# Performance work log

Hardware: AMD Instinct MI355X
Metric: run time of the kernel (lower is better)

Reference implementation:

```python
import jax, jax.numpy as jnp
import numpy as np

N = 50000
E = 800000
L = 0.7
EPS = 1e-12  # torch F.normalize eps


def setup_inputs() -> dict:
    key = jax.random.key(0)
    k1, k2, k3, k4, k5 = jax.random.split(key, 5)
    x = jax.random.normal(k1, (N, 256), dtype=jnp.float32)
    W = jax.random.normal(k2, (256, 128), dtype=jnp.float32) * 0.05
    b = jax.random.normal(k3, (128,), dtype=jnp.float32) * 0.05
    src = jax.random.randint(k4, (E,), 0, N, dtype=jnp.int32)
    dst = jax.random.randint(k5, (E,), 0, N, dtype=jnp.int32)
    return {"x": x, "W": W, "b": b, "src": src, "dst": dst}


def _mean_agg(h, src, dst, denom):
    # DGL copy_u + mean over in-edges: mean_{e:(u->v)} h[u]; zero for isolated nodes
    s = jax.ops.segment_sum(h[src], dst, num_segments=N)  # [N, D]
    return s / denom


def reference(x, W, b, src, dst):
    # MLP: Linear -> relu -> row-wise L2 normalize
    h = jax.nn.relu(x @ W + b)
    h = h / jnp.maximum(jnp.linalg.norm(h, axis=1, keepdims=True), EPS)
    # in-degree for mean (clamped to 1 so isolated nodes give 0, matching DGL)
    deg = jax.ops.segment_sum(jnp.ones((E,), jnp.float32), dst, num_segments=N)
    denom = jnp.maximum(deg, 1.0)[:, None]  # [N,1]
    neigh1 = _mean_agg(h, src, dst, denom)
    neigh2 = _mean_agg(neigh1, src, dst, denom)
    mean_h = L * neigh1 + (1.0 - L) * neigh2
    return (h, mean_h)
```

## Files before the change

### kernel.cpp

```cpp
#include <hip/hip_runtime.h>

#define D_IN 256
#define D_OUT 128
#define NBINS 256
#define NB 256

typedef short bf16x8 __attribute__((ext_vector_type(8)));
typedef float f32x4 __attribute__((ext_vector_type(4)));

__device__ __forceinline__ unsigned short f2bf(float f) {
    unsigned int u = __float_as_uint(f);
    unsigned int r = (u + 0x7FFFu + ((u >> 16) & 1u)) >> 16;
    return (unsigned short)r;
}
__device__ __forceinline__ unsigned int pack2(float a, float b) {
    return (unsigned int)f2bf(a) | ((unsigned int)f2bf(b) << 16);
}
__device__ __forceinline__ void gload_lds16(const void* g, void* l) {
    __builtin_amdgcn_global_load_lds(
        (const __attribute__((address_space(1))) void*)g,
        (__attribute__((address_space(3))) void*)l, 16, 0, 0);
}

__global__ __launch_bounds__(256) void k_wt_b1(const float* __restrict__ W,
                                               unsigned short* __restrict__ wt,
                                               const int* __restrict__ dst, int E, int epb,
                                               int* __restrict__ blockbase) {
    __shared__ int hist[NBINS];
    int t = threadIdx.x;
    if (t < 128) {
        int idx = blockIdx.x * 128 + t;
        wt[idx] = f2bf(W[(idx & 255) * D_OUT + (idx >> 8)]);
    }
    hist[t] = 0;
    __syncthreads();
    int s = blockIdx.x * epb;
    int e = min(s + epb, E);
    for (int i = s + t; i < e; i += 256)
        atomicAdd(&hist[dst[i] >> 8], 1);
    __syncthreads();
    blockbase[blockIdx.x * NBINS + t] = hist[t];
}

__global__ __launch_bounds__(256) void k_b2(int* __restrict__ blockbase,
                                            int* __restrict__ coarse_cnt,
                                            int* __restrict__ coarse_base) {
    __shared__ int sd[NBINS];
    int t = threadIdx.x;
    int run = 0;
    #pragma unroll 8
    for (int blk = 0; blk < NB; ++blk) {
        int v = blockbase[blk * NBINS + t];
        blockbase[blk * NBINS + t] = run;
        run += v;
    }
    coarse_cnt[t] = run;
    sd[t] = run;
    __syncthreads();
    for (int off = 1; off < 256; off <<= 1) {
        int v = (t >= off) ? sd[t - off] : 0;
        __syncthreads();
        sd[t] += v;
        __syncthreads();
    }
    coarse_base[t] = sd[t] - run;
}

__global__ __launch_bounds__(256) void k_b3(const int* __restrict__ src,
                                            const int* __restrict__ dst, int E, int epb,
                                            const int* __restrict__ coarse_base,
                                            const int* __restrict__ blockbase,
                                            int* __restrict__ ebuf) {
    __shared__ int cur[NBINS];
    int t = threadIdx.x;
    cur[t] = 0;
    __syncthreads();
    int s = blockIdx.x * epb;
    int e = min(s + epb, E);
    for (int i = s + t; i < e; i += 256) {
        int d = dst[i];
        int bin = d >> 8;
        int p = atomicAdd(&cur[bin], 1);
        int gpos = coarse_base[bin] + blockbase[blockIdx.x * NBINS + bin] + p;
        ebuf[gpos] = (src[i] & 0xffff) | ((d & 255) << 16);
    }
}

__global__ __launch_bounds__(256) void k_b4(const int* __restrict__ ebuf,
                                            const int* __restrict__ coarse_cnt,
                                            const int* __restrict__ coarse_base,
                                            int* __restrict__ deg, int* __restrict__ offs,
                                            int* __restrict__ csr, int n) {
    __shared__ int hist[NBINS];
    __shared__ int loffs[NBINS];
    int t = threadIdx.x;
    int bin = blockIdx.x;
    int base = coarse_base[bin];
    int size = coarse_cnt[bin];
    hist[t] = 0;
    __syncthreads();
    for (int i = t; i < size; i += 256)
        atomicAdd(&hist[(ebuf[base + i] >> 16) & 255], 1);
    __syncthreads();
    int h = hist[t];
    loffs[t] = h;
    __syncthreads();
    for (int off = 1; off < 256; off <<= 1) {
        int v = (t >= off) ? loffs[t - off] : 0;
        __syncthreads();
        loffs[t] += v;
        __syncthreads();
    }
    int excl = loffs[t] - h;
    int gdst = bin * 256 + t;
    if (gdst < n) {
        deg[gdst]  = h;
        offs[gdst] = base + excl;
    }
    __syncthreads();
    hist[t] = excl;
    __syncthreads();
    for (int i = t; i < size; i += 256) {
        int pr = ebuf[base + i];
        int p = atomicAdd(&hist[(pr >> 16) & 255], 1);
        csr[base + p] = pr & 0xffff;
    }
}

__global__ __launch_bounds__(256) void k_mlp(const float* __restrict__ x,
                                             const unsigned short* __restrict__ wt,
                                             const float* __restrict__ bias,
                                             float* __restrict__ h,
                                             unsigned char* __restrict__ hq, int n) {
    __shared__ float sx[64 * 64];
    __shared__ unsigned short swc[128 * 64];
    const int tid  = threadIdx.x;
    const int wid  = tid >> 6;
    const int lane = tid & 63;
    const int row0 = blockIdx.x * 64;

    f32x4 acc[8];
    #pragma unroll
    for (int fn = 0; fn < 8; ++fn) acc[fn] = (f32x4){0.f, 0.f, 0.f, 0.f};

    for (int k0 = 0; k0 < D_IN; k0 += 64) {
        __syncthreads();
        #pragma unroll
        for (int i = 0; i < 4; ++i) {
            int bi = i * 4 + wid;
            int chunk = bi * 64 + lane;
            int r  = chunk >> 4;
            int cs = chunk & 15;
            int grow = row0 + r;
            const float* g = x + (size_t)grow * D_IN + k0 + ((cs ^ (r & 7)) << 2);
            if (grow < n) gload_lds16(g, (char*)sx + bi * 1024);
        }
        #pragma unroll
        for (int i = 0; i < 4; ++i) {
            int bi = i * 4 + wid;
            int chunk = bi * 64 + lane;
            int nr = chunk >> 3;
            int cs = chunk & 7;
            const unsigned short* g = wt + nr * D_IN + k0 + ((cs ^ (nr & 7)) << 3);
            gload_lds16(g, (char*)swc + bi * 1024);
        }
        __syncthreads();

        #pragma unroll
        for (int kk = 0; kk < 2; ++kk) {
            int r  = wid * 16 + (lane & 15);
            int cs = kk * 8 + (lane >> 4) * 2;
            float4 a0 = *reinterpret_cast<const float4*>(sx + r * 64 + ((cs ^ (r & 7)) << 2));
            float4 a1 = *reinterpret_cast<const float4*>(sx + r * 64 + (((cs + 1) ^ (r & 7)) << 2));
            union { unsigned int u[4]; bf16x8 v; } af;
            af.u[0] = pack2(a0.x, a0.y);
            af.u[1] = pack2(a0.z, a0.w);
            af.u[2] = pack2(a1.x, a1.y);
            af.u[3] = pack2(a1.z, a1.w);
            #pragma unroll
            for (int fn = 0; fn < 8; ++fn) {
                int nr = fn * 16 + (lane & 15);
                int cb = kk * 4 + (lane >> 4);
                bf16x8 bfrag = *reinterpret_cast<const bf16x8*>(
                    swc + nr * 64 + ((cb ^ (nr & 7)) << 3));
                acc[fn] = __builtin_amdgcn_mfma_f32_16x16x32_bf16(af.v, bfrag, acc[fn], 0, 0, 0);
            }
        }
    }

    float bias_r[8];
    #pragma unroll
    for (int fn = 0; fn < 8; ++fn) bias_r[fn] = bias[fn * 16 + (lane & 15)];
    const int colbase = lane & 15;
    const int rgrp = lane >> 4;
    #pragma unroll
    for (int reg = 0; reg < 4; ++reg) {
        int grow = row0 + wid * 16 + rgrp * 4 + reg;
        float v[8];
        float ss = 0.f;
        #pragma unroll
        for (int fn = 0; fn < 8; ++fn) {
            float t = fmaxf(acc[fn][reg] + bias_r[fn], 0.f);
            v[fn] = t;
            ss += t * t;
        }
        ss += __shfl_xor(ss, 1);
        ss += __shfl_xor(ss, 2);
        ss += __shfl_xor(ss, 4);
        ss += __shfl_xor(ss, 8);
        float sc = 1.f / fmaxf(sqrtf(ss), 1e-12f);
        if (grow < n) {
            #pragma unroll
            for (int fn = 0; fn < 8; ++fn) {
                float o = v[fn] * sc;
                h[(size_t)grow * D_OUT + fn * 16 + colbase] = o;
                hq[(size_t)grow * D_OUT + fn * 16 + colbase] =
                    (unsigned char)(int)rintf(o * 255.f);
            }
        }
    }
}

__global__ __launch_bounds__(256) void k_agg1(const unsigned char* __restrict__ hq,
                                              const int* __restrict__ offs,
                                              const int* __restrict__ deg,
                                              const int* __restrict__ csr,
                                              unsigned char* __restrict__ n1q, int n) {
    int node = (blockIdx.x * blockDim.x + threadIdx.x) >> 5;
    int sub  = threadIdx.x & 31;
    if (node >= n) return;
    int d = deg[node];
    int s = offs[node], e = s + d;
    unsigned int a0 = 0u, a1 = 0u;
    int i = s;
    for (; i + 7 < e; i += 8) {
        #pragma unroll
        for (int j = 0; j < 8; ++j) {
            int u = csr[i + j];
            unsigned int q = *reinterpret_cast<const unsigned int*>(
                hq + (size_t)u * D_OUT + sub * 4);
            a0 += q & 0x00FF00FFu;
            a1 += (q >> 8) & 0x00FF00FFu;
        }
    }
    for (; i < e; ++i) {
        int u = csr[i];
        unsigned int q = *reinterpret_cast<const unsigned int*>(
            hq + (size_t)u * D_OUT + sub * 4);
        a0 += q & 0x00FF00FFu;
        a1 += (q >> 8) & 0x00FF00FFu;
    }
    float inv = 1.f / (float)max(d, 1);
    unsigned int b0 = (unsigned int)(int)rintf((float)(a0 & 0xffffu) * inv);
    unsigned int b1 = (unsigned int)(int)rintf((float)(a1 & 0xffffu) * inv);
    unsigned int b2 = (unsigned int)(int)rintf((float)(a0 >> 16) * inv);
    unsigned int b3 = (unsigned int)(int)rintf((float)(a1 >> 16) * inv);
    *reinterpret_cast<unsigned int*>(n1q + (size_t)node * D_OUT + sub * 4) =
        b0 | (b1 << 8) | (b2 << 16) | (b3 << 24);
}

__global__ __launch_bounds__(256) void k_agg2(const unsigned char* __restrict__ n1q,
                                              const int* __restrict__ offs,
                                              const int* __restrict__ deg,
                                              const int* __restrict__ csr,
                                              float* __restrict__ out_m, int n) {
    int node = (blockIdx.x * blockDim.x + threadIdx.x) >> 5;
    int sub  = threadIdx.x & 31;
    if (node >= n) return;
    int d = deg[node];
    int s = offs[node], e = s + d;
    unsigned int a0 = 0u, a1 = 0u;
    int i = s;
    for (; i + 7 < e; i += 8) {
        #pragma unroll
        for (int j = 0; j < 8; ++j) {
            int u = csr[i + j];
            unsigned int q = *reinterpret_cast<const unsigned int*>(
                n1q + (size_t)u * D_OUT + sub * 4);
            a0 += q & 0x00FF00FFu;
            a1 += (q >> 8) & 0x00FF00FFu;
        }
    }
    for (; i < e; ++i) {
        int u = csr[i];
        unsigned int q = *reinterpret_cast<const unsigned int*>(
            n1q + (size_t)u * D_OUT + sub * 4);
        a0 += q & 0x00FF00FFu;
        a1 += (q >> 8) & 0x00FF00FFu;
    }
    float inv = 1.f / (float)max(d, 1);
    unsigned int own = *reinterpret_cast<const unsigned int*>(
        n1q + (size_t)node * D_OUT + sub * 4);
    const float s255 = 1.f / 255.f;
    float4 o;
    o.x = (0.7f * (float)(own & 0xffu)         + 0.3f * (float)(a0 & 0xffffu) * inv) * s255;
    o.y = (0.7f * (float)((own >> 8) & 0xffu)  + 0.3f * (float)(a1 & 0xffffu) * inv) * s255;
    o.z = (0.7f * (float)((own >> 16) & 0xffu) + 0.3f * (float)(a0 >> 16) * inv) * s255;
    o.w = (0.7f * (float)(own >> 24)           + 0.3f * (float)(a1 >> 16) * inv) * s255;
    *reinterpret_cast<float4*>(out_m + (size_t)node * D_OUT + sub * 4) = o;
}

static inline size_t align_up(size_t v, size_t a) { return (v + a - 1) & ~(a - 1); }

extern "C" void kernel_launch(void* const* d_in, const int* in_sizes, int n_in,
                              void* d_out, int out_size, void* d_ws, size_t ws_size,
                              hipStream_t stream) {
    const float* x  = (const float*)d_in[0];
    const float* W  = (const float*)d_in[1];
    const float* b  = (const float*)d_in[2];
    const int* src  = (const int*)d_in[3];
    const int* dst  = (const int*)d_in[4];

    const int n = in_sizes[0] / D_IN;
    const int E = in_sizes[3];

    float* out_h = (float*)d_out;
    float* out_m = out_h + (size_t)n * D_OUT;

    char* ws = (char*)d_ws;
    size_t off = 0;
    int* coarse_cnt  = (int*)(ws + off); off = align_up(off + NBINS * 4, 256);
    int* coarse_base = (int*)(ws + off); off = align_up(off + NBINS * 4, 256);
    int* blockbase   = (int*)(ws + off); off = align_up(off + (size_t)NB * NBINS * 4, 256);
    int* ebuf        = (int*)(ws + off); off = align_up(off + (size_t)E * 4, 256);
    int* csr         = (int*)(ws + off); off = align_up(off + (size_t)E * 4, 256);
    int* deg         = (int*)(ws + off); off = align_up(off + (size_t)n * 4, 256);
    int* offs        = (int*)(ws + off); off = align_up(off + (size_t)n * 4, 256);
    unsigned short* wt = (unsigned short*)(ws + off); off = align_up(off + (size_t)D_OUT * D_IN * 2, 256);
    unsigned char* hq  = (unsigned char*)(ws + off); off = align_up(off + (size_t)n * D_OUT, 256);
    unsigned char* n1q = (unsigned char*)(ws + off); off = align_up(off + (size_t)n * D_OUT, 256);
    (void)ws_size;

    const int epb = (E + NB - 1) / NB;
    const int nbuckets = (n + 255) / 256;
    const int nmblk = (n + 63) / 64;

    k_wt_b1<<<NB, 256, 0, stream>>>(W, wt, dst, E, epb, blockbase);
    k_b2<<<1, 256, 0, stream>>>(blockbase, coarse_cnt, coarse_base);
    k_b3<<<NB, 256, 0, stream>>>(src, dst, E, epb, coarse_base, blockbase, ebuf);
    k_b4<<<nbuckets, 256, 0, stream>>>(ebuf, coarse_cnt, coarse_base, deg, offs, csr, n);

    k_mlp<<<nmblk, 256, 0, stream>>>(x, wt, b, out_h, hq, n);

    const int agg_nodes_per_block = 256 / 32;
    const int agg_blocks = (n + agg_nodes_per_block - 1) / agg_nodes_per_block;
    k_agg1<<<agg_blocks, 256, 0, stream>>>(hq, offs, deg, csr, n1q, n);
    k_agg2<<<agg_blocks, 256, 0, stream>>>(n1q, offs, deg, csr, out_m, n);
}
```

Measured before the change: 107.9 us.

## Fuse CSR build and MLP into one persistent kernel with grid barriers

Merges the four CSR-construction kernels and the MLP GEMM into a single launch. The first 240 blocks build the CSR using software grid barriers (atomic counters), and the remaining blocks run the MLP tiles concurrently. The MLP now converts W to bf16 inline on each load instead of using a pre-transposed workspace copy. The goal is to remove launch gaps and overlap graph preprocessing with the GEMM. In exchange it adds spin-wait barriers that rely on all 240 CSR blocks being co-resident, plus extra per-tile W conversion work.

```diff
diff --git a/kernel.cpp b/kernel.cpp
--- a/kernel.cpp
+++ b/kernel.cpp
@@ -3,7 +3,8 @@
 #define D_IN 256
 #define D_OUT 128
 #define NBINS 256
-#define NB 256
+#define NBC 240
+#define GRID_TOTAL 1024
 
 typedef short bf16x8 __attribute__((ext_vector_type(8)));
 typedef float f32x4 __attribute__((ext_vector_type(4)));
@@ -22,126 +23,134 @@
         (__attribute__((address_space(3))) void*)l, 16, 0, 0);
 }
 
-__global__ __launch_bounds__(256) void k_wt_b1(const float* __restrict__ W,
-                                               unsigned short* __restrict__ wt,
-                                               const int* __restrict__ dst, int E, int epb,
-                                               int* __restrict__ blockbase) {
-    __shared__ int hist[NBINS];
-    int t = threadIdx.x;
-    if (t < 128) {
-        int idx = blockIdx.x * 128 + t;
-        wt[idx] = f2bf(W[(idx & 255) * D_OUT + (idx >> 8)]);
-    }
-    hist[t] = 0;
+__device__ __forceinline__ void csr_barrier(int* cnt) {
     __syncthreads();
-    int s = blockIdx.x * epb;
-    int e = min(s + epb, E);
-    for (int i = s + t; i < e; i += 256)
-        atomicAdd(&hist[dst[i] >> 8], 1);
+    if (threadIdx.x == 0) {
+        __threadfence();
+        atomicAdd(cnt, 1);
+        while (atomicAdd(cnt, 0) < NBC) __builtin_amdgcn_s_sleep(8);
+        __threadfence();
+    }
     __syncthreads();
-    blockbase[blockIdx.x * NBINS + t] = hist[t];
-}
-
-__global__ __launch_bounds__(256) void k_b2(int* __restrict__ blockbase,
-                                            int* __restrict__ coarse_cnt,
-                                            int* __restrict__ coarse_base) {
-    __shared__ int sd[NBINS];
-    int t = threadIdx.x;
-    int run = 0;
-    #pragma unroll 8
-    for (int blk = 0; blk < NB; ++blk) {
-        int v = blockbase[blk * NBINS + t];
-        blockbase[blk * NBINS + t] = run;
-        run += v;
-    }
-    coarse_cnt[t] = run;
-    sd[t] = run;
-    __syncthreads();
-    for (int off = 1; off < 256; off <<= 1) {
-        int v = (t >= off) ? sd[t - off] : 0;
-        __syncthreads();
-        sd[t] += v;
-        __syncthreads();
-    }
-    coarse_base[t] = sd[t] - run;
-}
-
-__global__ __launch_bounds__(256) void k_b3(const int* __restrict__ src,
-                                            const int* __restrict__ dst, int E, int epb,
-                                            const int* __restrict__ coarse_base,
-                                            const int* __restrict__ blockbase,
-                                            int* __restrict__ ebuf) {
-    __shared__ int cur[NBINS];
-    int t = threadIdx.x;
-    cur[t] = 0;
-    __syncthreads();
-    int s = blockIdx.x * epb;
-    int e = min(s + epb, E);
-    for (int i = s + t; i < e; i += 256) {
-        int d = dst[i];
-        int bin = d >> 8;
-        int p = atomicAdd(&cur[bin], 1);
-        int gpos = coarse_base[bin] + blockbase[blockIdx.x * NBINS + bin] + p;
-        ebuf[gpos] = (src[i] & 0xffff) | ((d & 255) << 16);
-    }
-}
-
-__global__ __launch_bounds__(256) void k_b4(const int* __restrict__ ebuf,
-                                            const int* __restrict__ coarse_cnt,
-                                            const int* __restrict__ coarse_base,
-                                            int* __restrict__ deg, int* __restrict__ offs,
-                                            int* __restrict__ csr, int n) {
-    __shared__ int hist[NBINS];
-    __shared__ int loffs[NBINS];
-    int t = threadIdx.x;
-    int bin = blockIdx.x;
-    int base = coarse_base[bin];
-    int size = coarse_cnt[bin];
-    hist[t] = 0;
-    __syncthreads();
-    for (int i = t; i < size; i += 256)
-        atomicAdd(&hist[(ebuf[base + i] >> 16) & 255], 1);
-    __syncthreads();
-    int h = hist[t];
-    loffs[t] = h;
-    __syncthreads();
-    for (int off = 1; off < 256; off <<= 1) {
-        int v = (t >= off) ? loffs[t - off] : 0;
-        __syncthreads();
-        loffs[t] += v;
-        __syncthreads();
-    }
-    int excl = loffs[t] - h;
-    int gdst = bin * 256 + t;
-    if (gdst < n) {
-        deg[gdst]  = h;
-        offs[gdst] = base + excl;
-    }
-    __syncthreads();
-    hist[t] = excl;
-    __syncthreads();
-    for (int i = t; i < size; i += 256) {
-        int pr = ebuf[base + i];
-        int p = atomicAdd(&hist[(pr >> 16) & 255], 1);
-        csr[base + p] = pr & 0xffff;
-    }
-}
-
-__global__ __launch_bounds__(256) void k_mlp(const float* __restrict__ x,
-                                             const unsigned short* __restrict__ wt,
-                                             const float* __restrict__ bias,
-                                             float* __restrict__ h,
-                                             unsigned char* __restrict__ hq, int n) {
-    __shared__ float sx[64 * 64];
-    __shared__ unsigned short swc[128 * 64];
-    const int tid  = threadIdx.x;
+}
+
+__global__ __launch_bounds__(256, 4) void k_fused(
+    const float* __restrict__ x, const float* __restrict__ W,
+    const float* __restrict__ bias,
+    const int* __restrict__ src, const int* __restrict__ dst,
+    int E, int epb, int n, int nmblk,
+    int* __restrict__ blockbase, int* __restrict__ coarse_cnt,
+    int* __restrict__ coarse_base,
+    int* __restrict__ ebuf, int* __restrict__ deg, int* __restrict__ offs,
+    int* __restrict__ csr, float* __restrict__ h, unsigned char* __restrict__ hq,
+    int* __restrict__ bar) {
+    __shared__ char smem[32768];
+    const int tid = threadIdx.x;
+    const int bid = blockIdx.x;
+
+    if (bid < NBC) {
+        int* hist = (int*)smem;
+        hist[tid] = 0;
+        __syncthreads();
+        const int s = bid * epb, e = min(s + epb, E);
+        for (int i = s + tid; i < e; i += 256)
+            atomicAdd(&hist[dst[i] >> 8], 1);
+        __syncthreads();
+        blockbase[tid * NBC + bid] = hist[tid];
+        csr_barrier(&bar[0]);
+
+        int* sd = (int*)(smem + 1024);
+        for (int bin = bid; bin < NBINS; bin += NBC) {
+            int v = (tid < NBC) ? blockbase[bin * NBC + tid] : 0;
+            sd[tid] = v;
+            __syncthreads();
+            for (int off = 1; off < 256; off <<= 1) {
+                int t2 = (tid >= off) ? sd[tid - off] : 0;
+                __syncthreads();
+                sd[tid] += t2;
+                __syncthreads();
+            }
+            if (tid < NBC) blockbase[bin * NBC + tid] = sd[tid] - v;
+            if (tid == 255) coarse_cnt[bin] = sd[255];
+            __syncthreads();
+        }
+        csr_barrier(&bar[1]);
+
+        int* cur   = (int*)smem;
+        int* base  = (int*)(smem + 1024);
+        int* sd2   = (int*)(smem + 2048);
+        int cc = coarse_cnt[tid];
+        sd2[tid] = cc;
+        cur[tid] = 0;
+        __syncthreads();
+        for (int off = 1; off < 256; off <<= 1) {
+            int t2 = (tid >= off) ? sd2[tid - off] : 0;
+            __syncthreads();
+            sd2[tid] += t2;
+            __syncthreads();
+        }
+        int cb_excl = sd2[tid] - cc;
+        base[tid] = cb_excl + blockbase[tid * NBC + bid];
+        if (bid == 0) coarse_base[tid] = cb_excl;
+        __syncthreads();
+        for (int i = s + tid; i < e; i += 256) {
+            int d = dst[i];
+            int bin = d >> 8;
+            int p = atomicAdd(&cur[bin], 1);
+            ebuf[base[bin] + p] = (src[i] & 0xffff) | ((d & 255) << 16);
+        }
+        csr_barrier(&bar[2]);
+
+        const int nbuckets = (n + 255) / 256;
+        if (bid < nbuckets) {
+            int* h4 = (int*)smem;
+            int* lo = (int*)(smem + 1024);
+            const int bin = bid;
+            const int gbase = coarse_base[bin];
+            const int size = coarse_cnt[bin];
+            h4[tid] = 0;
+            __syncthreads();
+            for (int i = tid; i < size; i += 256)
+                atomicAdd(&h4[(ebuf[gbase + i] >> 16) & 255], 1);
+            __syncthreads();
+            int hh = h4[tid];
+            lo[tid] = hh;
+            __syncthreads();
+            for (int off = 1; off < 256; off <<= 1) {
+                int v = (tid >= off) ? lo[tid - off] : 0;
+                __syncthreads();
+                lo[tid] += v;
+                __syncthreads();
+            }
+            int excl = lo[tid] - hh;
+            int gdst = bin * 256 + tid;
+            if (gdst < n) { deg[gdst] = hh; offs[gdst] = gbase + excl; }
+            __syncthreads();
+            h4[tid] = excl;
+            __syncthreads();
+            for (int i = tid; i < size; i += 256) {
+                int pr = ebuf[gbase + i];
+                int p = atomicAdd(&h4[(pr >> 16) & 255], 1);
+                csr[gbase + p] = pr & 0xffff;
+            }
+        }
+        return;
+    }
+
+    const int tile = bid - NBC;
+    if (tile >= nmblk) return;
+    float* sx = (float*)smem;
+    unsigned short* swc = (unsigned short*)(smem + 16384);
     const int wid  = tid >> 6;
     const int lane = tid & 63;
-    const int row0 = blockIdx.x * 64;
+    const int row0 = tile * 64;
 
     f32x4 acc[8];
     #pragma unroll
     for (int fn = 0; fn < 8; ++fn) acc[fn] = (f32x4){0.f, 0.f, 0.f, 0.f};
+
+    const int nr_w  = tid & 127;
+    const int khalf = tid >> 7;
 
     for (int k0 = 0; k0 < D_IN; k0 += 64) {
         __syncthreads();
@@ -156,13 +165,24 @@
             if (grow < n) gload_lds16(g, (char*)sx + bi * 1024);
         }
         #pragma unroll
-        for (int i = 0; i < 4; ++i) {
-            int bi = i * 4 + wid;
-            int chunk = bi * 64 + lane;
-            int nr = chunk >> 3;
-            int cs = chunk & 7;
-            const unsigned short* g = wt + nr * D_IN + k0 + ((cs ^ (nr & 7)) << 3);
-            gload_lds16(g, (char*)swc + bi * 1024);
+        for (int r8 = 0; r8 < 4; ++r8) {
+            int kg  = r8 * 2 + khalf;
+            int kc0 = kg * 8;
+            float w0 = W[(k0 + kc0 + 0) * D_OUT + nr_w];
+            float w1 = W[(k0 + kc0 + 1) * D_OUT + nr_w];
+            float w2 = W[(k0 + kc0 + 2) * D_OUT + nr_w];
+            float w3 = W[(k0 + kc0 + 3) * D_OUT + nr_w];
+            float w4 = W[(k0 + kc0 + 4) * D_OUT + nr_w];
+            float w5 = W[(k0 + kc0 + 5) * D_OUT + nr_w];
+            float w6 = W[(k0 + kc0 + 6) * D_OUT + nr_w];
+            float w7 = W[(k0 + kc0 + 7) * D_OUT + nr_w];
+            uint4 pv;
+            pv.x = pack2(w0, w1);
+            pv.y = pack2(w2, w3);
+            pv.z = pack2(w4, w5);
+            pv.w = pack2(w6, w7);
+            *reinterpret_cast<uint4*>(
+                (char*)swc + nr_w * 128 + ((kg ^ (nr_w & 7)) << 4)) = pv;
         }
         __syncthreads();
 
@@ -319,31 +339,27 @@
 
     char* ws = (char*)d_ws;
     size_t off = 0;
+    int* bar         = (int*)(ws + off); off = align_up(off + 16, 256);
     int* coarse_cnt  = (int*)(ws + off); off = align_up(off + NBINS * 4, 256);
     int* coarse_base = (int*)(ws + off); off = align_up(off + NBINS * 4, 256);
-    int* blockbase   = (int*)(ws + off); off = align_up(off + (size_t)NB * NBINS * 4, 256);
+    int* blockbase   = (int*)(ws + off); off = align_up(off + (size_t)NBINS * NBC * 4, 256);
     int* ebuf        = (int*)(ws + off); off = align_up(off + (size_t)E * 4, 256);
     int* csr         = (int*)(ws + off); off = align_up(off + (size_t)E * 4, 256);
     int* deg         = (int*)(ws + off); off = align_up(off + (size_t)n * 4, 256);
     int* offs        = (int*)(ws + off); off = align_up(off + (size_t)n * 4, 256);
-    unsigned short* wt = (unsigned short*)(ws + off); off = align_up(off + (size_t)D_OUT * D_IN * 2, 256);
     unsigned char* hq  = (unsigned char*)(ws + off); off = align_up(off + (size_t)n * D_OUT, 256);
     unsigned char* n1q = (unsigned char*)(ws + off); off = align_up(off + (size_t)n * D_OUT, 256);
     (void)ws_size;
 
-    const int epb = (E + NB - 1) / NB;
-    const int nbuckets = (n + 255) / 256;
+    const int epb = (E + NBC - 1) / NBC;
     const int nmblk = (n + 63) / 64;
 
-    k_wt_b1<<<NB, 256, 0, stream>>>(W, wt, dst, E, epb, blockbase);
-    k_b2<<<1, 256, 0, stream>>>(blockbase, coarse_cnt, coarse_base);
-    k_b3<<<NB, 256, 0, stream>>>(src, dst, E, epb, coarse_base, blockbase, ebuf);
-    k_b4<<<nbuckets, 256, 0, stream>>>(ebuf, coarse_cnt, coarse_base, deg, offs, csr, n);
-
-    k_mlp<<<nmblk, 256, 0, stream>>>(x, wt, b, out_h, hq, n);
-
-    const int agg_nodes_per_block = 256 / 32;
-    const int agg_blocks = (n + agg_nodes_per_block - 1) / agg_nodes_per_block;
+    hipMemsetAsync(bar, 0, 16, stream);
+    k_fused<<<GRID_TOTAL, 256, 0, stream>>>(x, W, b, src, dst, E, epb, n, nmblk,
+                                            blockbase, coarse_cnt, coarse_base,
+                                            ebuf, deg, offs, csr, out_h, hq, bar);
+
+    const int agg_blocks = (n + 7) / 8;
     k_agg1<<<agg_blocks, 256, 0, stream>>>(hq, offs, deg, csr, n1q, n);
     k_agg2<<<agg_blocks, 256, 0, stream>>>(n1q, offs, deg, csr, out_m, n);
 }
```

After: 174.7 us. 62.0% more time.

## Fuse CSR bucket finalization with first mean aggregation into one kernel

Applied to the files above, without the earlier changes.

Merges the per-bucket CSR build kernel and the first aggregation kernel into a single 1024-thread block per 256-node bucket. Each block builds its local degree/offset/CSR slice in shared memory, then aggregates its 256 nodes directly, and the launch moves after the MLP. This removes one launch and avoids re-reading deg/offs from global memory. In exchange, only about 196 large blocks do the gather, which lowers parallelism and occupancy for the memory-bound aggregation.

```diff
diff --git a/kernel.cpp b/kernel.cpp
--- a/kernel.cpp
+++ b/kernel.cpp
@@ -83,47 +83,6 @@
         int p = atomicAdd(&cur[bin], 1);
         int gpos = coarse_base[bin] + blockbase[blockIdx.x * NBINS + bin] + p;
         ebuf[gpos] = (src[i] & 0xffff) | ((d & 255) << 16);
-    }
-}
-
-__global__ __launch_bounds__(256) void k_b4(const int* __restrict__ ebuf,
-                                            const int* __restrict__ coarse_cnt,
-                                            const int* __restrict__ coarse_base,
-                                            int* __restrict__ deg, int* __restrict__ offs,
-                                            int* __restrict__ csr, int n) {
-    __shared__ int hist[NBINS];
-    __shared__ int loffs[NBINS];
-    int t = threadIdx.x;
-    int bin = blockIdx.x;
-    int base = coarse_base[bin];
-    int size = coarse_cnt[bin];
-    hist[t] = 0;
-    __syncthreads();
-    for (int i = t; i < size; i += 256)
-        atomicAdd(&hist[(ebuf[base + i] >> 16) & 255], 1);
-    __syncthreads();
-    int h = hist[t];
-    loffs[t] = h;
-    __syncthreads();
-    for (int off = 1; off < 256; off <<= 1) {
-        int v = (t >= off) ? loffs[t - off] : 0;
-        __syncthreads();
-        loffs[t] += v;
-        __syncthreads();
-    }
-    int excl = loffs[t] - h;
-    int gdst = bin * 256 + t;
-    if (gdst < n) {
-        deg[gdst]  = h;
-        offs[gdst] = base + excl;
-    }
-    __syncthreads();
-    hist[t] = excl;
-    __syncthreads();
-    for (int i = t; i < size; i += 256) {
-        int pr = ebuf[base + i];
-        int p = atomicAdd(&hist[(pr >> 16) & 255], 1);
-        csr[base + p] = pr & 0xffff;
     }
 }
 
@@ -221,42 +180,86 @@
     }
 }
 
-__global__ __launch_bounds__(256) void k_agg1(const unsigned char* __restrict__ hq,
-                                              const int* __restrict__ offs,
-                                              const int* __restrict__ deg,
-                                              const int* __restrict__ csr,
-                                              unsigned char* __restrict__ n1q, int n) {
-    int node = (blockIdx.x * blockDim.x + threadIdx.x) >> 5;
-    int sub  = threadIdx.x & 31;
-    if (node >= n) return;
-    int d = deg[node];
-    int s = offs[node], e = s + d;
-    unsigned int a0 = 0u, a1 = 0u;
-    int i = s;
-    for (; i + 7 < e; i += 8) {
-        #pragma unroll
-        for (int j = 0; j < 8; ++j) {
-            int u = csr[i + j];
+__global__ __launch_bounds__(1024) void k_b4agg1(const int* __restrict__ ebuf,
+                                                 const int* __restrict__ coarse_cnt,
+                                                 const int* __restrict__ coarse_base,
+                                                 const unsigned char* __restrict__ hq,
+                                                 int* __restrict__ deg, int* __restrict__ offs,
+                                                 int* __restrict__ csr,
+                                                 unsigned char* __restrict__ n1q, int n) {
+    __shared__ int hist[NBINS];
+    __shared__ int lo[NBINS];
+    __shared__ int sdeg[NBINS];
+    __shared__ int soffs[NBINS];
+    const int t = threadIdx.x;
+    const int bin = blockIdx.x;
+    const int gbase = coarse_base[bin];
+    const int size = coarse_cnt[bin];
+
+    if (t < 256) hist[t] = 0;
+    __syncthreads();
+    for (int i = t; i < size; i += 1024)
+        atomicAdd(&hist[(ebuf[gbase + i] >> 16) & 255], 1);
+    __syncthreads();
+    int hh = 0;
+    if (t < 256) { hh = hist[t]; lo[t] = hh; }
+    __syncthreads();
+    for (int off = 1; off < 256; off <<= 1) {
+        int v = (t >= off && t < 256) ? lo[t - off] : 0;
+        __syncthreads();
+        if (t < 256) lo[t] += v;
+        __syncthreads();
+    }
+    if (t < 256) {
+        int excl = lo[t] - hh;
+        sdeg[t]  = hh;
+        soffs[t] = gbase + excl;
+        int gdst = bin * 256 + t;
+        if (gdst < n) { deg[gdst] = hh; offs[gdst] = soffs[t]; }
+        hist[t] = excl;
+    }
+    __syncthreads();
+    for (int i = t; i < size; i += 1024) {
+        int pr = ebuf[gbase + i];
+        int p = atomicAdd(&hist[(pr >> 16) & 255], 1);
+        csr[gbase + p] = pr & 0xffff;
+    }
+    __syncthreads();
+
+    const int hw = t >> 5;
+    const int sub = t & 31;
+    for (int nl = hw; nl < 256; nl += 32) {
+        int gdst = bin * 256 + nl;
+        if (gdst >= n) continue;
+        int d = sdeg[nl];
+        int s = soffs[nl], e = s + d;
+        unsigned int a0 = 0u, a1 = 0u;
+        int i = s;
+        for (; i + 7 < e; i += 8) {
+            #pragma unroll
+            for (int j = 0; j < 8; ++j) {
+                int u = csr[i + j];
+                unsigned int q = *reinterpret_cast<const unsigned int*>(
+                    hq + (size_t)u * D_OUT + sub * 4);
+                a0 += q & 0x00FF00FFu;
+                a1 += (q >> 8) & 0x00FF00FFu;
+            }
+        }
+        for (; i < e; ++i) {
+            int u = csr[i];
             unsigned int q = *reinterpret_cast<const unsigned int*>(
                 hq + (size_t)u * D_OUT + sub * 4);
             a0 += q & 0x00FF00FFu;
             a1 += (q >> 8) & 0x00FF00FFu;
         }
-    }
-    for (; i < e; ++i) {
-        int u = csr[i];
-        unsigned int q = *reinterpret_cast<const unsigned int*>(
-            hq + (size_t)u * D_OUT + sub * 4);
-        a0 += q & 0x00FF00FFu;
-        a1 += (q >> 8) & 0x00FF00FFu;
-    }
-    float inv = 1.f / (float)max(d, 1);
-    unsigned int b0 = (unsigned int)(int)rintf((float)(a0 & 0xffffu) * inv);
-    unsigned int b1 = (unsigned int)(int)rintf((float)(a1 & 0xffffu) * inv);
-    unsigned int b2 = (unsigned int)(int)rintf((float)(a0 >> 16) * inv);
-    unsigned int b3 = (unsigned int)(int)rintf((float)(a1 >> 16) * inv);
-    *reinterpret_cast<unsigned int*>(n1q + (size_t)node * D_OUT + sub * 4) =
-        b0 | (b1 << 8) | (b2 << 16) | (b3 << 24);
+        float inv = 1.f / (float)max(d, 1);
+        unsigned int b0 = (unsigned int)(int)rintf((float)(a0 & 0xffffu) * inv);
+        unsigned int b1 = (unsigned int)(int)rintf((float)(a1 & 0xffffu) * inv);
+        unsigned int b2 = (unsigned int)(int)rintf((float)(a0 >> 16) * inv);
+        unsigned int b3 = (unsigned int)(int)rintf((float)(a1 >> 16) * inv);
+        *reinterpret_cast<unsigned int*>(n1q + (size_t)gdst * D_OUT + sub * 4) =
+            b0 | (b1 << 8) | (b2 << 16) | (b3 << 24);
+    }
 }
 
 __global__ __launch_bounds__(256) void k_agg2(const unsigned char* __restrict__ n1q,
@@ -338,12 +341,13 @@
     k_wt_b1<<<NB, 256, 0, stream>>>(W, wt, dst, E, epb, blockbase);
     k_b2<<<1, 256, 0, stream>>>(blockbase, coarse_cnt, coarse_base);
     k_b3<<<NB, 256, 0, stream>>>(src, dst, E, epb, coarse_base, blockbase, ebuf);
-    k_b4<<<nbuckets, 256, 0, stream>>>(ebuf, coarse_cnt, coarse_base, deg, offs, csr, n);
 
     k_mlp<<<nmblk, 256, 0, stream>>>(x, wt, b, out_h, hq, n);
+
+    k_b4agg1<<<nbuckets, 1024, 0, stream>>>(ebuf, coarse_cnt, coarse_base, hq,
+                                            deg, offs, csr, n1q, n);
 
     const int agg_nodes_per_block = 256 / 32;
     const int agg_blocks = (n + agg_nodes_per_block - 1) / agg_nodes_per_block;
-    k_agg1<<<agg_blocks, 256, 0, stream>>>(hq, offs, deg, csr, n1q, n);
     k_agg2<<<agg_blocks, 256, 0, stream>>>(n1q, offs, deg, csr, out_m, n);
 }
```

Measured after the change: 113.9 us. +5.6%, slower.

## Fuse bucket scan and scatter into MLP kernel launch, drop single-block scan

Applied to the files above, without the earlier changes.

Removes the single-block prefix-scan kernel: each scatter block now computes its own per-bin prefix by scanning a transposed blockbase row (one row per thread), and also redoes the 256-bin coarse scan redundantly. The scatter blocks and the MLP tiles are merged into one heterogeneous launch so the edge bucketing overlaps with the GEMM. This cuts two launches and a serial one-block kernel, at the cost of redundant per-block scans and a larger combined shared-memory footprint for the scatter blocks.

```diff
diff --git a/kernel.cpp b/kernel.cpp
--- a/kernel.cpp
+++ b/kernel.cpp
@@ -39,105 +39,61 @@
     for (int i = s + t; i < e; i += 256)
         atomicAdd(&hist[dst[i] >> 8], 1);
     __syncthreads();
-    blockbase[blockIdx.x * NBINS + t] = hist[t];
-}
-
-__global__ __launch_bounds__(256) void k_b2(int* __restrict__ blockbase,
-                                            int* __restrict__ coarse_cnt,
-                                            int* __restrict__ coarse_base) {
-    __shared__ int sd[NBINS];
-    int t = threadIdx.x;
-    int run = 0;
-    #pragma unroll 8
-    for (int blk = 0; blk < NB; ++blk) {
-        int v = blockbase[blk * NBINS + t];
-        blockbase[blk * NBINS + t] = run;
-        run += v;
-    }
-    coarse_cnt[t] = run;
-    sd[t] = run;
-    __syncthreads();
-    for (int off = 1; off < 256; off <<= 1) {
-        int v = (t >= off) ? sd[t - off] : 0;
-        __syncthreads();
-        sd[t] += v;
-        __syncthreads();
-    }
-    coarse_base[t] = sd[t] - run;
-}
-
-__global__ __launch_bounds__(256) void k_b3(const int* __restrict__ src,
-                                            const int* __restrict__ dst, int E, int epb,
-                                            const int* __restrict__ coarse_base,
-                                            const int* __restrict__ blockbase,
-                                            int* __restrict__ ebuf) {
-    __shared__ int cur[NBINS];
-    int t = threadIdx.x;
-    cur[t] = 0;
-    __syncthreads();
-    int s = blockIdx.x * epb;
-    int e = min(s + epb, E);
-    for (int i = s + t; i < e; i += 256) {
-        int d = dst[i];
-        int bin = d >> 8;
-        int p = atomicAdd(&cur[bin], 1);
-        int gpos = coarse_base[bin] + blockbase[blockIdx.x * NBINS + bin] + p;
-        ebuf[gpos] = (src[i] & 0xffff) | ((d & 255) << 16);
-    }
-}
-
-__global__ __launch_bounds__(256) void k_b4(const int* __restrict__ ebuf,
-                                            const int* __restrict__ coarse_cnt,
-                                            const int* __restrict__ coarse_base,
-                                            int* __restrict__ deg, int* __restrict__ offs,
-                                            int* __restrict__ csr, int n) {
-    __shared__ int hist[NBINS];
-    __shared__ int loffs[NBINS];
-    int t = threadIdx.x;
-    int bin = blockIdx.x;
-    int base = coarse_base[bin];
-    int size = coarse_cnt[bin];
-    hist[t] = 0;
-    __syncthreads();
-    for (int i = t; i < size; i += 256)
-        atomicAdd(&hist[(ebuf[base + i] >> 16) & 255], 1);
-    __syncthreads();
-    int h = hist[t];
-    loffs[t] = h;
-    __syncthreads();
-    for (int off = 1; off < 256; off <<= 1) {
-        int v = (t >= off) ? loffs[t - off] : 0;
-        __syncthreads();
-        loffs[t] += v;
-        __syncthreads();
-    }
-    int excl = loffs[t] - h;
-    int gdst = bin * 256 + t;
-    if (gdst < n) {
-        deg[gdst]  = h;
-        offs[gdst] = base + excl;
-    }
-    __syncthreads();
-    hist[t] = excl;
-    __syncthreads();
-    for (int i = t; i < size; i += 256) {
-        int pr = ebuf[base + i];
-        int p = atomicAdd(&hist[(pr >> 16) & 255], 1);
-        csr[base + p] = pr & 0xffff;
-    }
-}
-
-__global__ __launch_bounds__(256) void k_mlp(const float* __restrict__ x,
-                                             const unsigned short* __restrict__ wt,
-                                             const float* __restrict__ bias,
-                                             float* __restrict__ h,
-                                             unsigned char* __restrict__ hq, int n) {
-    __shared__ float sx[64 * 64];
-    __shared__ unsigned short swc[128 * 64];
-    const int tid  = threadIdx.x;
+    blockbase[t * NB + blockIdx.x] = hist[t];
+}
+
+__global__ __launch_bounds__(256) void k_csrmlp(
+    const int* __restrict__ src, const int* __restrict__ dst, int E, int epb,
+    const int* __restrict__ blockbase, int* __restrict__ coarse_cnt,
+    int* __restrict__ coarse_base, int* __restrict__ ebuf,
+    const float* __restrict__ x, const unsigned short* __restrict__ wt,
+    const float* __restrict__ bias, float* __restrict__ h,
+    unsigned char* __restrict__ hq, int n, int nmblk) {
+    __shared__ char smem[32768];
+    const int tid = threadIdx.x;
+    const int bid = blockIdx.x;
+
+    if (bid < NB) {
+        int* cur  = (int*)smem;
+        int* base = (int*)(smem + 1024);
+        int* sd   = (int*)(smem + 2048);
+        const int* row = blockbase + tid * NB;
+        int run = 0, myprefix = 0;
+        #pragma unroll 8
+        for (int b = 0; b < NB; ++b) {
+            if (b == bid) myprefix = run;
+            run += row[b];
+        }
+        sd[tid] = run;
+        cur[tid] = 0;
+        __syncthreads();
+        for (int off = 1; off < 256; off <<= 1) {
+            int v = (tid >= off) ? sd[tid - off] : 0;
+            __syncthreads();
+            sd[tid] += v;
+            __syncthreads();
+        }
+        int cb_excl = sd[tid] - run;
+        base[tid] = cb_excl + myprefix;
+        if (bid == 0) { coarse_cnt[tid] = run; coarse_base[tid] = cb_excl; }
+        __syncthreads();
+        const int s = bid * epb, e = min(s + epb, E);
+        for (int i = s + tid; i < e; i += 256) {
+            int d = dst[i];
+            int bin = d >> 8;
+            int p = atomicAdd(&cur[bin], 1);
+            ebuf[base[bin] + p] = (src[i] & 0xffff) | ((d & 255) << 16);
+        }
+        return;
+    }
+
+    const int tile = bid - NB;
+    if (tile >= nmblk) return;
+    float* sx = (float*)smem;
+    unsigned short* swc = (unsigned short*)(smem + 16384);
     const int wid  = tid >> 6;
     const int lane = tid & 63;
-    const int row0 = blockIdx.x * 64;
+    const int row0 = tile * 64;
 
     f32x4 acc[8];
     #pragma unroll
@@ -221,6 +177,47 @@
     }
 }
 
+__global__ __launch_bounds__(256) void k_b4(const int* __restrict__ ebuf,
+                                            const int* __restrict__ coarse_cnt,
+                                            const int* __restrict__ coarse_base,
+                                            int* __restrict__ deg, int* __restrict__ offs,
+                                            int* __restrict__ csr, int n) {
+    __shared__ int hist[NBINS];
+    __shared__ int loffs[NBINS];
+    int t = threadIdx.x;
+    int bin = blockIdx.x;
+    int base = coarse_base[bin];
+    int size = coarse_cnt[bin];
+    hist[t] = 0;
+    __syncthreads();
+    for (int i = t; i < size; i += 256)
+        atomicAdd(&hist[(ebuf[base + i] >> 16) & 255], 1);
+    __syncthreads();
+    int h = hist[t];
+    loffs[t] = h;
+    __syncthreads();
+    for (int off = 1; off < 256; off <<= 1) {
+        int v = (t >= off) ? loffs[t - off] : 0;
+        __syncthreads();
+        loffs[t] += v;
+        __syncthreads();
+    }
+    int excl = loffs[t] - h;
+    int gdst = bin * 256 + t;
+    if (gdst < n) {
+        deg[gdst]  = h;
+        offs[gdst] = base + excl;
+    }
+    __syncthreads();
+    hist[t] = excl;
+    __syncthreads();
+    for (int i = t; i < size; i += 256) {
+        int pr = ebuf[base + i];
+        int p = atomicAdd(&hist[(pr >> 16) & 255], 1);
+        csr[base + p] = pr & 0xffff;
+    }
+}
+
 __global__ __launch_bounds__(256) void k_agg1(const unsigned char* __restrict__ hq,
                                               const int* __restrict__ offs,
                                               const int* __restrict__ deg,
@@ -321,7 +318,7 @@
     size_t off = 0;
     int* coarse_cnt  = (int*)(ws + off); off = align_up(off + NBINS * 4, 256);
     int* coarse_base = (int*)(ws + off); off = align_up(off + NBINS * 4, 256);
-    int* blockbase   = (int*)(ws + off); off = align_up(off + (size_t)NB * NBINS * 4, 256);
+    int* blockbase   = (int*)(ws + off); off = align_up(off + (size_t)NBINS * NB * 4, 256);
     int* ebuf        = (int*)(ws + off); off = align_up(off + (size_t)E * 4, 256);
     int* csr         = (int*)(ws + off); off = align_up(off + (size_t)E * 4, 256);
     int* deg         = (int*)(ws + off); off = align_up(off + (size_t)n * 4, 256);
@@ -336,14 +333,12 @@
     const int nmblk = (n + 63) / 64;
 
     k_wt_b1<<<NB, 256, 0, stream>>>(W, wt, dst, E, epb, blockbase);
-    k_b2<<<1, 256, 0, stream>>>(blockbase, coarse_cnt, coarse_base);
-    k_b3<<<NB, 256, 0, stream>>>(src, dst, E, epb, coarse_base, blockbase, ebuf);
+    k_csrmlp<<<NB + nmblk, 256, 0, stream>>>(src, dst, E, epb, blockbase,
+                                             coarse_cnt, coarse_base, ebuf,
+                                             x, wt, b, out_h, hq, n, nmblk);
     k_b4<<<nbuckets, 256, 0, stream>>>(ebuf, coarse_cnt, coarse_base, deg, offs, csr, n);
 
-    k_mlp<<<nmblk, 256, 0, stream>>>(x, wt, b, out_h, hq, n);
-
-    const int agg_nodes_per_block = 256 / 32;
-    const int agg_blocks = (n + agg_nodes_per_block - 1) / agg_nodes_per_block;
+    const int agg_blocks = (n + 7) / 8;
     k_agg1<<<agg_blocks, 256, 0, stream>>>(hq, offs, deg, csr, n1q, n);
     k_agg2<<<agg_blocks, 256, 0, stream>>>(n1q, offs, deg, csr, out_m, n);
 }
```

After: 97.69 us. 1.1x faster.
